# Optimization experiments

Hardware: AMD Instinct MI355X
Metric: run time of the kernel (lower is better)

## Reference

```python
import jax, jax.numpy as jnp
import numpy as np

HEADS = 4
DIM_HEAD = 32
SCALE = DIM_HEAD ** -0.5
EPS = 1e-5


def setup_inputs() -> dict:
    key = jax.random.key(0)
    ks = jax.random.split(key, 4)
    B, C, H, W = 16, 128, 32, 32
    hid = HEADS * DIM_HEAD  # 128
    return {
        "x": jax.random.normal(ks[0], (B, C, H, W), jnp.float32),
        "gn_weight": jnp.ones((C,), jnp.float32),
        "gn_bias": jnp.zeros((C,), jnp.float32),
        "w_qkv": jax.random.normal(ks[1], (3 * hid, C), jnp.float32) * 0.05,  # 1x1 conv, no bias
        "w_out": jax.random.normal(ks[2], (C, hid), jnp.float32) * 0.05,      # 1x1 conv
        "b_out": jax.random.normal(ks[3], (C,), jnp.float32) * 0.05,
    }


def reference(x, gn_weight, gn_bias, w_qkv, w_out, b_out):
    B, C, H, W = x.shape
    N = H * W
    # GroupNorm(num_groups=1): normalize over (C, H, W) per sample, per-channel affine
    mu = x.mean(axis=(1, 2, 3), keepdims=True)
    var = x.var(axis=(1, 2, 3), keepdims=True)
    xn = (x - mu) * jax.lax.rsqrt(var + EPS)
    xn = xn * gn_weight[None, :, None, None] + gn_bias[None, :, None, None]

    xf = xn.reshape(B, C, N)  # b c n
    qkv = jnp.einsum('bcn,oc->bon', xf, w_qkv)  # 1x1 conv == matmul over channels
    q, k, v = jnp.split(qkv, 3, axis=1)

    def to_heads(t):  # 'b (h c) x y -> b h (x y) c'
        return t.reshape(B, HEADS, DIM_HEAD, N).transpose(0, 1, 3, 2)  # b h n c

    q, k, v = map(to_heads, (q, k, v))

    q = jax.nn.softmax(q, axis=-2) * SCALE  # softmax over spatial tokens
    k = jax.nn.softmax(k, axis=-1)          # softmax over channel dim

    # Faithful to source einsums: contract over CHANNEL dim -> (b, h, N, N) context
    context = jnp.einsum('bhdc,bhec->bhde', k, v)      # b h n n
    out = jnp.einsum('bhde,bhdc->bhec', context, q)    # b h n c

    # 'b h (x y) c -> b (h c) x y'
    outf = out.transpose(0, 1, 3, 2).reshape(B, HEADS * DIM_HEAD, N)
    y = jnp.einsum('bcn,oc->bon', outf, w_out) + b_out[None, :, None]
    return y.reshape(B, C, H, W)
```

## Files before the change

kernel.cpp:

```cpp
#include <hip/hip_runtime.h>
#include <math.h>

#define CIN 128
#define NTOK 1024
#define SCALE_Q 0.17677669529663687f
#define GN_EPS 1e-5f
#define PB (CIN * NTOK)

#define WS_WQKVB 0
#define WS_PSTATS 24576
#define WS_PQSUM 25088
#define WS_VST 57856
#define WS_PM 1106432

typedef __bf16 bf16x8 __attribute__((ext_vector_type(8)));
typedef float f32x4 __attribute__((ext_vector_type(4)));

__device__ __forceinline__ unsigned short f2bf(float f) {
    union { float f; unsigned u; } v; v.f = f;
    unsigned r = v.u + 0x7fffu + ((v.u >> 16) & 1u);
    return (unsigned short)(r >> 16);
}
__device__ __forceinline__ unsigned pack2(float a, float b) {
    return (unsigned)f2bf(a) | ((unsigned)f2bf(b) << 16);
}

__global__ __launch_bounds__(256) void k_pre(const float* __restrict__ x,
                                             const float* __restrict__ wqkv,
                                             float* __restrict__ ws) {
    float* pstats = ws + WS_PSTATS;
    unsigned short* wqkvb = (unsigned short*)(ws + WS_WQKVB);
    __shared__ float sD[8];
    int bid = blockIdx.x, t = threadIdx.x;
    int lane = t & 63, wave = t >> 6;
    const float4* p = (const float4*)(x + (size_t)bid * 8192);
    float s = 0.f, s2 = 0.f;
    #pragma unroll
    for (int i = 0; i < 8; i++) {
        float4 v = p[t + 256 * i];
        s += v.x + v.y + v.z + v.w;
        s2 += v.x * v.x + v.y * v.y + v.z * v.z + v.w * v.w;
    }
    #pragma unroll
    for (int off = 32; off; off >>= 1) {
        s += __shfl_down(s, off);
        s2 += __shfl_down(s2, off);
    }
    if (lane == 0) { sD[wave * 2] = s; sD[wave * 2 + 1] = s2; }
    if (bid < 48) {
        float4 v = ((const float4*)(wqkv + bid * 1024))[t];
        uint2 pk2; pk2.x = pack2(v.x, v.y); pk2.y = pack2(v.z, v.w);
        *(uint2*)(wqkvb + bid * 1024 + t * 4) = pk2;
    }
    __syncthreads();
    if (t == 0) {
        pstats[bid * 2] = sD[0] + sD[2] + sD[4] + sD[6];
        pstats[bid * 2 + 1] = sD[1] + sD[3] + sD[5] + sD[7];
    }
}

__global__ __launch_bounds__(256, 1) void k_qkvm(const float* __restrict__ x,
                                                 const float* __restrict__ gw,
                                                 const float* __restrict__ gb,
                                                 float* __restrict__ ws) {
    __shared__ __align__(16) char smem[71680];
    unsigned short (*Al)[136] = (unsigned short(*)[136])smem;
    float (*Xl)[68] = (float(*)[68])(smem + 17408);
    unsigned short (*Bl)[136] = (unsigned short(*)[136])(smem + 17408);
    unsigned short (*kTl)[72] = (unsigned short(*)[72])(smem + 17408);
    unsigned short (*qTl)[72] = (unsigned short(*)[72])(smem + 52224);
    unsigned short (*Vl)[136] = (unsigned short(*)[136])(smem + 52224);
    float* sD = (float*)(smem + 70656);

    unsigned short* wqkvb = (unsigned short*)(ws + WS_WQKVB);
    float* pstats = ws + WS_PSTATS;
    float* pqsum = ws + WS_PQSUM;
    unsigned short* Vst = (unsigned short*)(ws + WS_VST);
    float* pM = ws + WS_PM;

    int bid = blockIdx.x, t = threadIdx.x;
    int b = bid >> 4, nt = bid & 15;
    int lane = t & 63, wave = t >> 6;
    int l15 = lane & 15, lk = (lane >> 4) * 8;
    int wn0 = (wave & 1) * 32, wo0 = (wave >> 1) * 64;

    if (t < 32) sD[t] = pstats[b * 32 + t];
    __syncthreads();
    float mu, rsv;
    {
        float s = 0.f, s2 = 0.f;
        #pragma unroll
        for (int i = 0; i < 16; i++) { s += sD[2 * i]; s2 += sD[2 * i + 1]; }
        mu = s * (1.f / PB);
        float var = s2 * (1.f / PB) - mu * mu;
        rsv = rsqrtf(var + GN_EPS);
    }
    {
        int c = t >> 1, hf = t & 1;
        float g = gw[c] * rsv, bb = gb[c] - mu * g;
        const float4* src = (const float4*)(x + ((size_t)b * CIN + c) * NTOK + nt * 64 + hf * 32);
        #pragma unroll
        for (int i = 0; i < 8; i++) {
            float4 v = src[i];
            float4 r = { v.x * g + bb, v.y * g + bb, v.z * g + bb, v.w * g + bb };
            *(float4*)&Xl[c][hf * 32 + i * 4] = r;
        }
    }
    __syncthreads();
    {
        int n = t & 63, kq = (t >> 6) * 32;
        unsigned pk[16];
        #pragma unroll
        for (int j = 0; j < 16; j++) pk[j] = pack2(Xl[kq + 2 * j][n], Xl[kq + 2 * j + 1][n]);
        #pragma unroll
        for (int j = 0; j < 4; j++) *(uint4*)(&Al[n][kq] + j * 8) = *(uint4*)(pk + j * 4);
    }
    __syncthreads();

    f32x4 qacc[2][4] = {}, kacc[2][4] = {};
    {
        int row = t >> 1, hf = t & 1;
        const uint4* src = (const uint4*)(wqkvb + (size_t)row * CIN + hf * 64);
        uint4* dst = (uint4*)&Bl[row][hf * 64];
        #pragma unroll
        for (int j = 0; j < 8; j++) dst[j] = src[j];
    }
    __syncthreads();
    #pragma unroll
    for (int ks = 0; ks < 4; ks++) {
        bf16x8 av[2], bv[4];
        #pragma unroll
        for (int i = 0; i < 2; i++) av[i] = *(const bf16x8*)&Al[wn0 + i * 16 + l15][ks * 32 + lk];
        #pragma unroll
        for (int j = 0; j < 4; j++) bv[j] = *(const bf16x8*)&Bl[wo0 + j * 16 + l15][ks * 32 + lk];
        #pragma unroll
        for (int i = 0; i < 2; i++)
            #pragma unroll
            for (int j = 0; j < 4; j++)
                qacc[i][j] = __builtin_amdgcn_mfma_f32_16x16x32_bf16(av[i], bv[j], qacc[i][j], 0, 0, 0);
    }
    __syncthreads();
    {
        int row = t >> 1, hf = t & 1;
        const uint4* src = (const uint4*)(wqkvb + (size_t)(128 + row) * CIN + hf * 64);
        uint4* dst = (uint4*)&Bl[row][hf * 64];
        #pragma unroll
        for (int j = 0; j < 8; j++) dst[j] = src[j];
    }
    __syncthreads();
    #pragma unroll
    for (int ks = 0; ks < 4; ks++) {
        bf16x8 av[2], bv[4];
        #pragma unroll
        for (int i = 0; i < 2; i++) av[i] = *(const bf16x8*)&Al[wn0 + i * 16 + l15][ks * 32 + lk];
        #pragma unroll
        for (int j = 0; j < 4; j++) bv[j] = *(const bf16x8*)&Bl[wo0 + j * 16 + l15][ks * 32 + lk];
        #pragma unroll
        for (int i = 0; i < 2; i++)
            #pragma unroll
            for (int j = 0; j < 4; j++)
                kacc[i][j] = __builtin_amdgcn_mfma_f32_16x16x32_bf16(av[i], bv[j], kacc[i][j], 0, 0, 0);
    }
    __syncthreads();

    float eq[2][4][4], ek[2][4][4];
    #pragma unroll
    for (int i = 0; i < 2; i++)
        #pragma unroll
        for (int j = 0; j < 4; j++)
            #pragma unroll
            for (int r = 0; r < 4; r++) {
                eq[i][j][r] = __expf(qacc[i][j][r]);
                ek[i][j][r] = __expf(kacc[i][j][r]);
            }
    #pragma unroll
    for (int i = 0; i < 2; i++)
        #pragma unroll
        for (int r = 0; r < 4; r++) {
            float e01 = ek[i][0][r] + ek[i][1][r];
            float e23 = ek[i][2][r] + ek[i][3][r];
            #pragma unroll
            for (int m = 1; m < 16; m <<= 1) {
                e01 += __shfl_xor(e01, m);
                e23 += __shfl_xor(e23, m);
            }
            float i01 = 1.f / e01, i23 = 1.f / e23;
            ek[i][0][r] *= i01; ek[i][1][r] *= i01;
            ek[i][2][r] *= i23; ek[i][3][r] *= i23;
        }
    #pragma unroll
    for (int i = 0; i < 2; i++)
        #pragma unroll
        for (int j = 0; j < 4; j++) {
            int ch = wo0 + j * 16 + l15;
            int tokb = wn0 + i * 16 + (lane >> 4) * 4;
            *(unsigned*)&kTl[ch][tokb] = pack2(ek[i][j][0], ek[i][j][1]);
            *(unsigned*)&kTl[ch][tokb + 2] = pack2(ek[i][j][2], ek[i][j][3]);
            *(unsigned*)&qTl[ch][tokb] = pack2(eq[i][j][0], eq[i][j][1]);
            *(unsigned*)&qTl[ch][tokb + 2] = pack2(eq[i][j][2], eq[i][j][3]);
        }
    #pragma unroll
    for (int j = 0; j < 4; j++) {
        float sq = 0.f;
        #pragma unroll
        for (int i = 0; i < 2; i++)
            #pragma unroll
            for (int r = 0; r < 4; r++) sq += eq[i][j][r];
        sq += __shfl_xor(sq, 16);
        sq += __shfl_xor(sq, 32);
        if (lane < 16) sD[(wave & 1) * 128 + wo0 + j * 16 + lane] = sq;
    }
    __syncthreads();
    if (t < 128) pqsum[(size_t)bid * 128 + t] = sD[t] + sD[128 + t];
    {
        f32x4 mac[2][2] = {};
        #pragma unroll
        for (int ks = 0; ks < 2; ks++) {
            bf16x8 av[2], bv[2];
            #pragma unroll
            for (int i = 0; i < 2; i++) av[i] = *(const bf16x8*)&kTl[wave * 32 + i * 16 + l15][ks * 32 + lk];
            #pragma unroll
            for (int j = 0; j < 2; j++) bv[j] = *(const bf16x8*)&qTl[wave * 32 + j * 16 + l15][ks * 32 + lk];
            #pragma unroll
            for (int i = 0; i < 2; i++)
                #pragma unroll
                for (int j = 0; j < 2; j++)
                    mac[i][j] = __builtin_amdgcn_mfma_f32_16x16x32_bf16(av[i], bv[j], mac[i][j], 0, 0, 0);
        }
        float* pmb = pM + ((size_t)bid * 4 + wave) * 1024;
        #pragma unroll
        for (int i = 0; i < 2; i++)
            #pragma unroll
            for (int j = 0; j < 2; j++)
                #pragma unroll
                for (int r = 0; r < 4; r++)
                    pmb[(i * 16 + (lane >> 4) * 4 + r) * 32 + j * 16 + l15] = mac[i][j][r];
    }
    __syncthreads();

    {
        int row = t >> 1, hf = t & 1;
        const uint4* src = (const uint4*)(wqkvb + (size_t)(256 + row) * CIN + hf * 64);
        uint4* dst = (uint4*)&Bl[row][hf * 64];
        #pragma unroll
        for (int j = 0; j < 8; j++) dst[j] = src[j];
    }
    __syncthreads();
    f32x4 vacc[2][4] = {};
    #pragma unroll
    for (int ks = 0; ks < 4; ks++) {
        bf16x8 av[2], bv[4];
        #pragma unroll
        for (int i = 0; i < 2; i++) av[i] = *(const bf16x8*)&Al[wn0 + i * 16 + l15][ks * 32 + lk];
        #pragma unroll
        for (int j = 0; j < 4; j++) bv[j] = *(const bf16x8*)&Bl[wo0 + j * 16 + l15][ks * 32 + lk];
        #pragma unroll
        for (int i = 0; i < 2; i++)
            #pragma unroll
            for (int j = 0; j < 4; j++)
                vacc[i][j] = __builtin_amdgcn_mfma_f32_16x16x32_bf16(av[i], bv[j], vacc[i][j], 0, 0, 0);
    }
    #pragma unroll
    for (int i = 0; i < 2; i++)
        #pragma unroll
        for (int j = 0; j < 4; j++) {
            int ch = wo0 + j * 16 + l15;
            #pragma unroll
            for (int r = 0; r < 4; r++)
                Vl[wn0 + i * 16 + (lane >> 4) * 4 + r][ch] = f2bf(vacc[i][j][r]);
        }
    __syncthreads();
    {
        int row = t >> 2, q = t & 3;
        const uint4* src = (const uint4*)&Vl[row][q * 32];
        uint4* dst = (uint4*)(Vst + ((size_t)bid * 64 + row) * CIN + q * 32);
        #pragma unroll
        for (int j = 0; j < 4; j++) dst[j] = src[j];
    }
}

__global__ __launch_bounds__(256, 1) void k_out(const float* __restrict__ wout,
                                                const float* __restrict__ bout,
                                                float* __restrict__ ws,
                                                float* __restrict__ y) {
    __shared__ __align__(16) char smem[80384];
    unsigned short (*Wl)[136] = (unsigned short(*)[136])smem;
    unsigned short (*Ul)[136] = (unsigned short(*)[136])(smem + 34816);
    unsigned short (*Vl)[136] = (unsigned short(*)[136])(smem + 52224);
    unsigned short (*Mt)[32][40] = (unsigned short(*)[32][40])(smem + 69632);
    float* sD = (float*)(smem + 79872);

    float* pqsum = ws + WS_PQSUM;
    unsigned short* Vst = (unsigned short*)(ws + WS_VST);
    float* pM = ws + WS_PM;

    int bid = blockIdx.x, t = threadIdx.x;
    int b = bid >> 4, nt = bid & 15;
    int lane = t & 63, wave = t >> 6;
    int l15 = lane & 15, lk = (lane >> 4) * 8;
    int wn0 = (wave & 1) * 32, wo0 = (wave >> 1) * 64;

    if (t < 128) {
        float s = 0.f;
        #pragma unroll
        for (int i = 0; i < 16; i++) s += pqsum[((size_t)(b * 16 + i)) * 128 + t];
        sD[t] = SCALE_Q / s;
    }
    {
        int row = t >> 2, q = t & 3;
        const uint4* src = (const uint4*)(Vst + ((size_t)bid * 64 + row) * CIN + q * 32);
        uint4* dst = (uint4*)&Vl[row][q * 32];
        #pragma unroll
        for (int j = 0; j < 4; j++) dst[j] = src[j];
    }
    #pragma unroll
    for (int s4 = 0; s4 < 4; s4++) {
        int slot = t + (s4 << 8);
        int h = slot >> 8, cp = (slot >> 3) & 31, c4 = slot & 7;
        float4 m = { 0.f, 0.f, 0.f, 0.f };
        for (int i = 0; i < 16; i++) {
            const float4 v = *(const float4*)&pM[(((size_t)(b * 16 + i)) * 4 + h) * 1024 + cp * 32 + c4 * 4];
            m.x += v.x; m.y += v.y; m.z += v.z; m.w += v.w;
        }
        Mt[h][c4 * 4 + 0][cp] = f2bf(m.x);
        Mt[h][c4 * 4 + 1][cp] = f2bf(m.y);
        Mt[h][c4 * 4 + 2][cp] = f2bf(m.z);
        Mt[h][c4 * 4 + 3][cp] = f2bf(m.w);
    }
    __syncthreads();

    f32x4 uac[4][2] = {};
    {
        bf16x8 mv[2];
        #pragma unroll
        for (int j = 0; j < 2; j++) mv[j] = *(const bf16x8*)&Mt[wave][j * 16 + l15][lk];
        #pragma unroll
        for (int i = 0; i < 4; i++) {
            bf16x8 av = *(const bf16x8*)&Vl[i * 16 + l15][wave * 32 + lk];
            #pragma unroll
            for (int j = 0; j < 2; j++)
                uac[i][j] = __builtin_amdgcn_mfma_f32_16x16x32_bf16(av, mv[j], uac[i][j], 0, 0, 0);
        }
    }
    {
        int o = t >> 1, hf = t & 1;
        const float4* src = (const float4*)(wout + (size_t)o * CIN + hf * 64);
        unsigned pk[32];
        #pragma unroll
        for (int i = 0; i < 16; i++) {
            float4 v = src[i];
            int c = hf * 64 + i * 4;
            v.x *= sD[c]; v.y *= sD[c + 1]; v.z *= sD[c + 2]; v.w *= sD[c + 3];
            pk[2 * i] = pack2(v.x, v.y);
            pk[2 * i + 1] = pack2(v.z, v.w);
        }
        uint4* dst = (uint4*)&Wl[o][hf * 64];
        #pragma unroll
        for (int j = 0; j < 8; j++) dst[j] = *(uint4*)(pk + j * 4);
    }
    #pragma unroll
    for (int i = 0; i < 4; i++)
        #pragma unroll
        for (int j = 0; j < 2; j++) {
            int ch = wave * 32 + j * 16 + l15;
            #pragma unroll
            for (int r = 0; r < 4; r++)
                Ul[i * 16 + (lane >> 4) * 4 + r][ch] = f2bf(uac[i][j][r]);
        }
    __syncthreads();

    f32x4 yacc[4][2] = {};
    #pragma unroll
    for (int ks = 0; ks < 4; ks++) {
        bf16x8 av[4], bv[2];
        #pragma unroll
        for (int i = 0; i < 4; i++) av[i] = *(const bf16x8*)&Wl[wo0 + i * 16 + l15][ks * 32 + lk];
        #pragma unroll
        for (int j = 0; j < 2; j++) bv[j] = *(const bf16x8*)&Ul[wn0 + j * 16 + l15][ks * 32 + lk];
        #pragma unroll
        for (int i = 0; i < 4; i++)
            #pragma unroll
            for (int j = 0; j < 2; j++)
                yacc[i][j] = __builtin_amdgcn_mfma_f32_16x16x32_bf16(av[i], bv[j], yacc[i][j], 0, 0, 0);
    }
    #pragma unroll
    for (int i = 0; i < 4; i++)
        #pragma unroll
        for (int r = 0; r < 4; r++) {
            int o = wo0 + i * 16 + (lane >> 4) * 4 + r;
            float bias = bout[o];
            float* yp = y + ((size_t)b * CIN + o) * NTOK + nt * 64 + wn0;
            #pragma unroll
            for (int j = 0; j < 2; j++) yp[j * 16 + l15] = yacc[i][j][r] + bias;
        }
}

extern "C" void kernel_launch(void* const* d_in, const int* in_sizes, int n_in,
                              void* d_out, int out_size, void* d_ws, size_t ws_size,
                              hipStream_t stream) {
    const float* x = (const float*)d_in[0];
    const float* gw = (const float*)d_in[1];
    const float* gb = (const float*)d_in[2];
    const float* wqkv = (const float*)d_in[3];
    const float* wout = (const float*)d_in[4];
    const float* bout = (const float*)d_in[5];
    float* y = (float*)d_out;
    float* ws = (float*)d_ws;

    k_pre<<<dim3(256), 256, 0, stream>>>(x, wqkv, ws);
    k_qkvm<<<dim3(256), 256, 0, stream>>>(x, gw, gb, ws);
    k_out<<<dim3(256), 256, 0, stream>>>(wout, bout, ws, y);
}
```

Before: 93.52 us.

## Double block size to 512 threads and compute Q and K projections concurrently

Both the QKV/context kernel and the output kernel now launch 512 threads per block instead of 256. In k_qkvm, the Q and K weights go into shared memory together, so eight waves compute both projections in one MFMA pass instead of two serial passes. The V-weight load by the upper waves now overlaps the per-head context matmul done by the lower waves. The output kernel splits its per-wave tiles in half. This aims to raise per-CU wave parallelism and remove serialized phases, at the cost of more shared memory (about 122 KB) and a larger register and sync footprint per block.

```diff
diff --git a/kernel.cpp b/kernel.cpp
--- a/kernel.cpp
+++ b/kernel.cpp
@@ -59,18 +59,18 @@
     }
 }
 
-__global__ __launch_bounds__(256, 1) void k_qkvm(const float* __restrict__ x,
+__global__ __launch_bounds__(512, 1) void k_qkvm(const float* __restrict__ x,
                                                  const float* __restrict__ gw,
                                                  const float* __restrict__ gb,
                                                  float* __restrict__ ws) {
-    __shared__ __align__(16) char smem[71680];
+    __shared__ __align__(16) char smem[124928];
     unsigned short (*Al)[136] = (unsigned short(*)[136])smem;
+    unsigned short (*Bl)[136] = (unsigned short(*)[136])(smem + 17408);
     float (*Xl)[68] = (float(*)[68])(smem + 17408);
-    unsigned short (*Bl)[136] = (unsigned short(*)[136])(smem + 17408);
-    unsigned short (*kTl)[72] = (unsigned short(*)[72])(smem + 17408);
-    unsigned short (*qTl)[72] = (unsigned short(*)[72])(smem + 52224);
-    unsigned short (*Vl)[136] = (unsigned short(*)[136])(smem + 52224);
-    float* sD = (float*)(smem + 70656);
+    unsigned short (*kTl)[72] = (unsigned short(*)[72])(smem + 87040);
+    unsigned short (*Vl)[136] = (unsigned short(*)[136])(smem + 87040);
+    unsigned short (*qTl)[72] = (unsigned short(*)[72])(smem + 105472);
+    float* sD = (float*)(smem + 123904);
 
     unsigned short* wqkvb = (unsigned short*)(ws + WS_WQKVB);
     float* pstats = ws + WS_PSTATS;
@@ -82,7 +82,8 @@
     int b = bid >> 4, nt = bid & 15;
     int lane = t & 63, wave = t >> 6;
     int l15 = lane & 15, lk = (lane >> 4) * 8;
-    int wn0 = (wave & 1) * 32, wo0 = (wave >> 1) * 64;
+    int sel = wave >> 1;
+    int wn0 = (wave & 1) * 32;
 
     if (t < 32) sD[t] = pstats[b * 32 + t];
     __syncthreads();
@@ -96,28 +97,26 @@
         rsv = rsqrtf(var + GN_EPS);
     }
     {
-        int c = t >> 1, hf = t & 1;
+        int c = t >> 2, qtr = t & 3;
         float g = gw[c] * rsv, bb = gb[c] - mu * g;
-        const float4* src = (const float4*)(x + ((size_t)b * CIN + c) * NTOK + nt * 64 + hf * 32);
-        #pragma unroll
-        for (int i = 0; i < 8; i++) {
+        const float4* src = (const float4*)(x + ((size_t)b * CIN + c) * NTOK + nt * 64 + qtr * 16);
+        #pragma unroll
+        for (int i = 0; i < 4; i++) {
             float4 v = src[i];
             float4 r = { v.x * g + bb, v.y * g + bb, v.z * g + bb, v.w * g + bb };
-            *(float4*)&Xl[c][hf * 32 + i * 4] = r;
-        }
-    }
-    __syncthreads();
-    {
-        int n = t & 63, kq = (t >> 6) * 32;
-        unsigned pk[16];
-        #pragma unroll
-        for (int j = 0; j < 16; j++) pk[j] = pack2(Xl[kq + 2 * j][n], Xl[kq + 2 * j + 1][n]);
-        #pragma unroll
-        for (int j = 0; j < 4; j++) *(uint4*)(&Al[n][kq] + j * 8) = *(uint4*)(pk + j * 4);
-    }
-    __syncthreads();
-
-    f32x4 qacc[2][4] = {}, kacc[2][4] = {};
+            *(float4*)&Xl[c][qtr * 16 + i * 4] = r;
+        }
+    }
+    __syncthreads();
+    {
+        int n = t & 63, kq = (t >> 6) * 16;
+        unsigned pk[8];
+        #pragma unroll
+        for (int j = 0; j < 8; j++) pk[j] = pack2(Xl[kq + 2 * j][n], Xl[kq + 2 * j + 1][n]);
+        *(uint4*)&Al[n][kq] = *(uint4*)pk;
+        *(uint4*)(&Al[n][kq] + 8) = *(uint4*)(pk + 4);
+    }
+    __syncthreads();
     {
         int row = t >> 1, hf = t & 1;
         const uint4* src = (const uint4*)(wqkvb + (size_t)row * CIN + hf * 64);
@@ -126,108 +125,97 @@
         for (int j = 0; j < 8; j++) dst[j] = src[j];
     }
     __syncthreads();
+
+    f32x4 acc[2][4] = {};
     #pragma unroll
     for (int ks = 0; ks < 4; ks++) {
         bf16x8 av[2], bv[4];
         #pragma unroll
         for (int i = 0; i < 2; i++) av[i] = *(const bf16x8*)&Al[wn0 + i * 16 + l15][ks * 32 + lk];
         #pragma unroll
-        for (int j = 0; j < 4; j++) bv[j] = *(const bf16x8*)&Bl[wo0 + j * 16 + l15][ks * 32 + lk];
+        for (int j = 0; j < 4; j++) bv[j] = *(const bf16x8*)&Bl[sel * 64 + j * 16 + l15][ks * 32 + lk];
         #pragma unroll
         for (int i = 0; i < 2; i++)
             #pragma unroll
             for (int j = 0; j < 4; j++)
-                qacc[i][j] = __builtin_amdgcn_mfma_f32_16x16x32_bf16(av[i], bv[j], qacc[i][j], 0, 0, 0);
-    }
-    __syncthreads();
-    {
-        int row = t >> 1, hf = t & 1;
-        const uint4* src = (const uint4*)(wqkvb + (size_t)(128 + row) * CIN + hf * 64);
-        uint4* dst = (uint4*)&Bl[row][hf * 64];
-        #pragma unroll
-        for (int j = 0; j < 8; j++) dst[j] = src[j];
-    }
-    __syncthreads();
-    #pragma unroll
-    for (int ks = 0; ks < 4; ks++) {
-        bf16x8 av[2], bv[4];
-        #pragma unroll
-        for (int i = 0; i < 2; i++) av[i] = *(const bf16x8*)&Al[wn0 + i * 16 + l15][ks * 32 + lk];
-        #pragma unroll
-        for (int j = 0; j < 4; j++) bv[j] = *(const bf16x8*)&Bl[wo0 + j * 16 + l15][ks * 32 + lk];
-        #pragma unroll
-        for (int i = 0; i < 2; i++)
-            #pragma unroll
-            for (int j = 0; j < 4; j++)
-                kacc[i][j] = __builtin_amdgcn_mfma_f32_16x16x32_bf16(av[i], bv[j], kacc[i][j], 0, 0, 0);
-    }
-    __syncthreads();
-
-    float eq[2][4][4], ek[2][4][4];
+                acc[i][j] = __builtin_amdgcn_mfma_f32_16x16x32_bf16(av[i], bv[j], acc[i][j], 0, 0, 0);
+    }
+
+    float e[2][4][4];
     #pragma unroll
     for (int i = 0; i < 2; i++)
         #pragma unroll
         for (int j = 0; j < 4; j++)
             #pragma unroll
+            for (int r = 0; r < 4; r++) e[i][j][r] = __expf(acc[i][j][r]);
+
+    if (sel >= 2) {
+        #pragma unroll
+        for (int i = 0; i < 2; i++)
+            #pragma unroll
             for (int r = 0; r < 4; r++) {
-                eq[i][j][r] = __expf(qacc[i][j][r]);
-                ek[i][j][r] = __expf(kacc[i][j][r]);
+                float e01 = e[i][0][r] + e[i][1][r];
+                float e23 = e[i][2][r] + e[i][3][r];
+                #pragma unroll
+                for (int m = 1; m < 16; m <<= 1) {
+                    e01 += __shfl_xor(e01, m);
+                    e23 += __shfl_xor(e23, m);
+                }
+                float i01 = 1.f / e01, i23 = 1.f / e23;
+                e[i][0][r] *= i01; e[i][1][r] *= i01;
+                e[i][2][r] *= i23; e[i][3][r] *= i23;
             }
-    #pragma unroll
-    for (int i = 0; i < 2; i++)
-        #pragma unroll
-        for (int r = 0; r < 4; r++) {
-            float e01 = ek[i][0][r] + ek[i][1][r];
-            float e23 = ek[i][2][r] + ek[i][3][r];
-            #pragma unroll
-            for (int m = 1; m < 16; m <<= 1) {
-                e01 += __shfl_xor(e01, m);
-                e23 += __shfl_xor(e23, m);
+        #pragma unroll
+        for (int i = 0; i < 2; i++)
+            #pragma unroll
+            for (int j = 0; j < 4; j++) {
+                int ch = (sel - 2) * 64 + j * 16 + l15;
+                int tokb = wn0 + i * 16 + (lane >> 4) * 4;
+                *(unsigned*)&kTl[ch][tokb] = pack2(e[i][j][0], e[i][j][1]);
+                *(unsigned*)&kTl[ch][tokb + 2] = pack2(e[i][j][2], e[i][j][3]);
             }
-            float i01 = 1.f / e01, i23 = 1.f / e23;
-            ek[i][0][r] *= i01; ek[i][1][r] *= i01;
-            ek[i][2][r] *= i23; ek[i][3][r] *= i23;
-        }
-    #pragma unroll
-    for (int i = 0; i < 2; i++)
+    } else {
+        #pragma unroll
+        for (int i = 0; i < 2; i++)
+            #pragma unroll
+            for (int j = 0; j < 4; j++) {
+                int ch = sel * 64 + j * 16 + l15;
+                int tokb = wn0 + i * 16 + (lane >> 4) * 4;
+                *(unsigned*)&qTl[ch][tokb] = pack2(e[i][j][0], e[i][j][1]);
+                *(unsigned*)&qTl[ch][tokb + 2] = pack2(e[i][j][2], e[i][j][3]);
+            }
         #pragma unroll
         for (int j = 0; j < 4; j++) {
-            int ch = wo0 + j * 16 + l15;
-            int tokb = wn0 + i * 16 + (lane >> 4) * 4;
-            *(unsigned*)&kTl[ch][tokb] = pack2(ek[i][j][0], ek[i][j][1]);
-            *(unsigned*)&kTl[ch][tokb + 2] = pack2(ek[i][j][2], ek[i][j][3]);
-            *(unsigned*)&qTl[ch][tokb] = pack2(eq[i][j][0], eq[i][j][1]);
-            *(unsigned*)&qTl[ch][tokb + 2] = pack2(eq[i][j][2], eq[i][j][3]);
-        }
-    #pragma unroll
-    for (int j = 0; j < 4; j++) {
-        float sq = 0.f;
-        #pragma unroll
-        for (int i = 0; i < 2; i++)
-            #pragma unroll
-            for (int r = 0; r < 4; r++) sq += eq[i][j][r];
-        sq += __shfl_xor(sq, 16);
-        sq += __shfl_xor(sq, 32);
-        if (lane < 16) sD[(wave & 1) * 128 + wo0 + j * 16 + lane] = sq;
+            float sq = 0.f;
+            #pragma unroll
+            for (int i = 0; i < 2; i++)
+                #pragma unroll
+                for (int r = 0; r < 4; r++) sq += e[i][j][r];
+            sq += __shfl_xor(sq, 16);
+            sq += __shfl_xor(sq, 32);
+            if (lane < 16) sD[(wave & 1) * 128 + sel * 64 + j * 16 + lane] = sq;
+        }
     }
     __syncthreads();
     if (t < 128) pqsum[(size_t)bid * 128 + t] = sD[t] + sD[128 + t];
-    {
+
+    if (wave < 4) {
+        int h = wave;
         f32x4 mac[2][2] = {};
         #pragma unroll
         for (int ks = 0; ks < 2; ks++) {
             bf16x8 av[2], bv[2];
             #pragma unroll
-            for (int i = 0; i < 2; i++) av[i] = *(const bf16x8*)&kTl[wave * 32 + i * 16 + l15][ks * 32 + lk];
-            #pragma unroll
-            for (int j = 0; j < 2; j++) bv[j] = *(const bf16x8*)&qTl[wave * 32 + j * 16 + l15][ks * 32 + lk];
+            for (int i = 0; i < 2; i++) av[i] = *(const bf16x8*)&kTl[h * 32 + i * 16 + l15][ks * 32 + lk];
+            #pragma unroll
+            for (int j = 0; j < 2; j++) bv[j] = *(const bf16x8*)&qTl[h * 32 + j * 16 + l15][ks * 32 + lk];
             #pragma unroll
             for (int i = 0; i < 2; i++)
                 #pragma unroll
                 for (int j = 0; j < 2; j++)
                     mac[i][j] = __builtin_amdgcn_mfma_f32_16x16x32_bf16(av[i], bv[j], mac[i][j], 0, 0, 0);
         }
-        float* pmb = pM + ((size_t)bid * 4 + wave) * 1024;
+        float* pmb = pM + ((size_t)bid * 4 + h) * 1024;
         #pragma unroll
         for (int i = 0; i < 2; i++)
             #pragma unroll
@@ -235,51 +223,52 @@
                 #pragma unroll
                 for (int r = 0; r < 4; r++)
                     pmb[(i * 16 + (lane >> 4) * 4 + r) * 32 + j * 16 + l15] = mac[i][j][r];
-    }
-    __syncthreads();
-
-    {
-        int row = t >> 1, hf = t & 1;
+    } else {
+        int t2 = t - 256;
+        int row = t2 >> 1, hf = t2 & 1;
         const uint4* src = (const uint4*)(wqkvb + (size_t)(256 + row) * CIN + hf * 64);
         uint4* dst = (uint4*)&Bl[row][hf * 64];
         #pragma unroll
         for (int j = 0; j < 8; j++) dst[j] = src[j];
     }
     __syncthreads();
-    f32x4 vacc[2][4] = {};
-    #pragma unroll
-    for (int ks = 0; ks < 4; ks++) {
-        bf16x8 av[2], bv[4];
-        #pragma unroll
-        for (int i = 0; i < 2; i++) av[i] = *(const bf16x8*)&Al[wn0 + i * 16 + l15][ks * 32 + lk];
-        #pragma unroll
-        for (int j = 0; j < 4; j++) bv[j] = *(const bf16x8*)&Bl[wo0 + j * 16 + l15][ks * 32 + lk];
-        #pragma unroll
-        for (int i = 0; i < 2; i++)
-            #pragma unroll
-            for (int j = 0; j < 4; j++)
-                vacc[i][j] = __builtin_amdgcn_mfma_f32_16x16x32_bf16(av[i], bv[j], vacc[i][j], 0, 0, 0);
-    }
-    #pragma unroll
-    for (int i = 0; i < 2; i++)
-        #pragma unroll
-        for (int j = 0; j < 4; j++) {
-            int ch = wo0 + j * 16 + l15;
-            #pragma unroll
-            for (int r = 0; r < 4; r++)
-                Vl[wn0 + i * 16 + (lane >> 4) * 4 + r][ch] = f2bf(vacc[i][j][r]);
-        }
-    __syncthreads();
-    {
-        int row = t >> 2, q = t & 3;
-        const uint4* src = (const uint4*)&Vl[row][q * 32];
-        uint4* dst = (uint4*)(Vst + ((size_t)bid * 64 + row) * CIN + q * 32);
-        #pragma unroll
-        for (int j = 0; j < 4; j++) dst[j] = src[j];
-    }
-}
-
-__global__ __launch_bounds__(256, 1) void k_out(const float* __restrict__ wout,
+
+    {
+        int wo0v = sel * 32;
+        f32x4 vacc[2][2] = {};
+        #pragma unroll
+        for (int ks = 0; ks < 4; ks++) {
+            bf16x8 av[2], bv[2];
+            #pragma unroll
+            for (int i = 0; i < 2; i++) av[i] = *(const bf16x8*)&Al[wn0 + i * 16 + l15][ks * 32 + lk];
+            #pragma unroll
+            for (int j = 0; j < 2; j++) bv[j] = *(const bf16x8*)&Bl[wo0v + j * 16 + l15][ks * 32 + lk];
+            #pragma unroll
+            for (int i = 0; i < 2; i++)
+                #pragma unroll
+                for (int j = 0; j < 2; j++)
+                    vacc[i][j] = __builtin_amdgcn_mfma_f32_16x16x32_bf16(av[i], bv[j], vacc[i][j], 0, 0, 0);
+        }
+        #pragma unroll
+        for (int i = 0; i < 2; i++)
+            #pragma unroll
+            for (int j = 0; j < 2; j++) {
+                int ch = wo0v + j * 16 + l15;
+                #pragma unroll
+                for (int r = 0; r < 4; r++)
+                    Vl[wn0 + i * 16 + (lane >> 4) * 4 + r][ch] = f2bf(vacc[i][j][r]);
+            }
+    }
+    __syncthreads();
+    {
+        int row = t >> 3, qq = t & 7;
+        uint4* dst = (uint4*)(Vst + ((size_t)bid * 64 + row) * CIN + qq * 16);
+        dst[0] = *(uint4*)&Vl[row][qq * 16];
+        dst[1] = *(uint4*)&Vl[row][qq * 16 + 8];
+    }
+}
+
+__global__ __launch_bounds__(512, 1) void k_out(const float* __restrict__ wout,
                                                 const float* __restrict__ bout,
                                                 float* __restrict__ ws,
                                                 float* __restrict__ y) {
@@ -298,7 +287,7 @@
     int b = bid >> 4, nt = bid & 15;
     int lane = t & 63, wave = t >> 6;
     int l15 = lane & 15, lk = (lane >> 4) * 8;
-    int wn0 = (wave & 1) * 32, wo0 = (wave >> 1) * 64;
+    int wn0 = (wave & 1) * 32;
 
     if (t < 128) {
         float s = 0.f;
@@ -307,15 +296,14 @@
         sD[t] = SCALE_Q / s;
     }
     {
-        int row = t >> 2, q = t & 3;
-        const uint4* src = (const uint4*)(Vst + ((size_t)bid * 64 + row) * CIN + q * 32);
-        uint4* dst = (uint4*)&Vl[row][q * 32];
-        #pragma unroll
-        for (int j = 0; j < 4; j++) dst[j] = src[j];
-    }
-    #pragma unroll
-    for (int s4 = 0; s4 < 4; s4++) {
-        int slot = t + (s4 << 8);
+        int row = t >> 3, qq = t & 7;
+        const uint4* src = (const uint4*)(Vst + ((size_t)bid * 64 + row) * CIN + qq * 16);
+        *(uint4*)&Vl[row][qq * 16] = src[0];
+        *(uint4*)&Vl[row][qq * 16 + 8] = src[1];
+    }
+    #pragma unroll
+    for (int s4 = 0; s4 < 2; s4++) {
+        int slot = t + (s4 << 9);
         int h = slot >> 8, cp = (slot >> 3) & 31, c4 = slot & 7;
         float4 m = { 0.f, 0.f, 0.f, 0.f };
         for (int i = 0; i < 16; i++) {
@@ -329,62 +317,64 @@
     }
     __syncthreads();
 
-    f32x4 uac[4][2] = {};
+    int head = wave >> 1;
+    f32x4 uac[2][2] = {};
     {
         bf16x8 mv[2];
         #pragma unroll
-        for (int j = 0; j < 2; j++) mv[j] = *(const bf16x8*)&Mt[wave][j * 16 + l15][lk];
-        #pragma unroll
-        for (int i = 0; i < 4; i++) {
-            bf16x8 av = *(const bf16x8*)&Vl[i * 16 + l15][wave * 32 + lk];
+        for (int j = 0; j < 2; j++) mv[j] = *(const bf16x8*)&Mt[head][j * 16 + l15][lk];
+        #pragma unroll
+        for (int i = 0; i < 2; i++) {
+            bf16x8 av = *(const bf16x8*)&Vl[wn0 + i * 16 + l15][head * 32 + lk];
             #pragma unroll
             for (int j = 0; j < 2; j++)
                 uac[i][j] = __builtin_amdgcn_mfma_f32_16x16x32_bf16(av, mv[j], uac[i][j], 0, 0, 0);
         }
     }
     {
-        int o = t >> 1, hf = t & 1;
-        const float4* src = (const float4*)(wout + (size_t)o * CIN + hf * 64);
-        unsigned pk[32];
-        #pragma unroll
-        for (int i = 0; i < 16; i++) {
+        int o = t >> 2, qtr = t & 3;
+        const float4* src = (const float4*)(wout + (size_t)o * CIN + qtr * 32);
+        unsigned pk[16];
+        #pragma unroll
+        for (int i = 0; i < 8; i++) {
             float4 v = src[i];
-            int c = hf * 64 + i * 4;
+            int c = qtr * 32 + i * 4;
             v.x *= sD[c]; v.y *= sD[c + 1]; v.z *= sD[c + 2]; v.w *= sD[c + 3];
             pk[2 * i] = pack2(v.x, v.y);
             pk[2 * i + 1] = pack2(v.z, v.w);
         }
-        uint4* dst = (uint4*)&Wl[o][hf * 64];
-        #pragma unroll
-        for (int j = 0; j < 8; j++) dst[j] = *(uint4*)(pk + j * 4);
-    }
-    #pragma unroll
-    for (int i = 0; i < 4; i++)
+        uint4* dst = (uint4*)&Wl[o][qtr * 32];
+        #pragma unroll
+        for (int j = 0; j < 4; j++) dst[j] = *(uint4*)(pk + j * 4);
+    }
+    #pragma unroll
+    for (int i = 0; i < 2; i++)
         #pragma unroll
         for (int j = 0; j < 2; j++) {
-            int ch = wave * 32 + j * 16 + l15;
+            int ch = head * 32 + j * 16 + l15;
             #pragma unroll
             for (int r = 0; r < 4; r++)
-                Ul[i * 16 + (lane >> 4) * 4 + r][ch] = f2bf(uac[i][j][r]);
-        }
-    __syncthreads();
-
-    f32x4 yacc[4][2] = {};
+                Ul[wn0 + i * 16 + (lane >> 4) * 4 + r][ch] = f2bf(uac[i][j][r]);
+        }
+    __syncthreads();
+
+    int wo0 = (wave >> 1) * 32;
+    f32x4 yacc[2][2] = {};
     #pragma unroll
     for (int ks = 0; ks < 4; ks++) {
-        bf16x8 av[4], bv[2];
-        #pragma unroll
-        for (int i = 0; i < 4; i++) av[i] = *(const bf16x8*)&Wl[wo0 + i * 16 + l15][ks * 32 + lk];
+        bf16x8 av[2], bv[2];
+        #pragma unroll
+        for (int i = 0; i < 2; i++) av[i] = *(const bf16x8*)&Wl[wo0 + i * 16 + l15][ks * 32 + lk];
         #pragma unroll
         for (int j = 0; j < 2; j++) bv[j] = *(const bf16x8*)&Ul[wn0 + j * 16 + l15][ks * 32 + lk];
         #pragma unroll
-        for (int i = 0; i < 4; i++)
+        for (int i = 0; i < 2; i++)
             #pragma unroll
             for (int j = 0; j < 2; j++)
                 yacc[i][j] = __builtin_amdgcn_mfma_f32_16x16x32_bf16(av[i], bv[j], yacc[i][j], 0, 0, 0);
     }
     #pragma unroll
-    for (int i = 0; i < 4; i++)
+    for (int i = 0; i < 2; i++)
         #pragma unroll
         for (int r = 0; r < 4; r++) {
             int o = wo0 + i * 16 + (lane >> 4) * 4 + r;
@@ -408,6 +398,6 @@
     float* ws = (float*)d_ws;
 
     k_pre<<<dim3(256), 256, 0, stream>>>(x, wqkv, ws);
-    k_qkvm<<<dim3(256), 256, 0, stream>>>(x, gw, gb, ws);
-    k_out<<<dim3(256), 256, 0, stream>>>(wout, bout, ws, y);
-}
+    k_qkvm<<<dim3(256), 512, 0, stream>>>(x, gw, gb, ws);
+    k_out<<<dim3(256), 512, 0, stream>>>(wout, bout, ws, y);
+}
```

After: 92.90 us. Within noise of the previous version (-0.7%).
